# Kernel optimization log

Hardware: AMD Instinct MI355X
Metric: run time of the kernel (lower is better)

## Reference

```python
import jax, jax.numpy as jnp
import numpy as np

N_NODES = 50000


def gcn_conv(x, src, dst, W, b):
    # PyG GCNConv: h = D^-1/2 (A+I) D^-1/2 (x W) + b, aggregation at dst.
    n = x.shape[0]
    deg = jax.ops.segment_sum(jnp.ones_like(dst, dtype=x.dtype), dst, num_segments=n)
    dinv = jnp.where(deg > 0, jax.lax.rsqrt(deg), 0.0)
    norm = dinv[src] * dinv[dst]                      # [E]
    h = x @ W                                         # [N, out]
    msg = h[src] * norm[:, None]                      # [E, out] gather
    out = jax.ops.segment_sum(msg, dst, num_segments=n)  # scatter-add
    return out + b


def setup_inputs() -> dict:
    key = jax.random.key(0)
    k1, k2, k3, k4 = jax.random.split(key, 4)
    in_dim, hid, out_dim = 128, 256, 128
    x = jax.random.normal(k1, (N_NODES, in_dim), dtype=jnp.float32)
    edge_index = jax.random.randint(k2, (2, 800000), 0, N_NODES, dtype=jnp.int64)
    s1 = 1.0 / np.sqrt(in_dim)
    s2 = 1.0 / np.sqrt(hid)
    W1 = jax.random.uniform(k3, (in_dim, hid), jnp.float32, -s1, s1)
    b1 = jnp.zeros((hid,), jnp.float32)
    W2 = jax.random.uniform(k4, (hid, out_dim), jnp.float32, -s2, s2)
    b2 = jnp.zeros((out_dim,), jnp.float32)
    return {"x": x, "edge_index": edge_index, "W1": W1, "b1": b1, "W2": W2, "b2": b2}


def reference(x, edge_index, W1, b1, W2, b2):
    n = x.shape[0]
    loops = jnp.arange(n, dtype=edge_index.dtype)
    src = jnp.concatenate([edge_index[0], loops])  # add self-loops
    dst = jnp.concatenate([edge_index[1], loops])
    h = jax.nn.relu(gcn_conv(x, src, dst, W1, b1))
    # dropout in eval mode -> identity
    return gcn_conv(h, src, dst, W2, b2)
```

## Files before the change

### kernel.cpp

```cpp
#include <hip/hip_runtime.h>
#include <hip/hip_bf16.h>


typedef __bf16 bf16x8v __attribute__((ext_vector_type(8)));
typedef short  s16x8   __attribute__((ext_vector_type(8)));
typedef float  f32x4   __attribute__((ext_vector_type(4)));

#define IN_DIM 128
#define HID    256
#define OUTD   128
#define BKT_SHIFT 7
#define BKT_NODES 128
#define MAXB 512
#define CAP  8192
#define EBLK 512

__device__ __forceinline__ float2 bf2f(__hip_bfloat162 v) {
    return make_float2(__bfloat162float(v.x), __bfloat162float(v.y));
}
__device__ __forceinline__ __hip_bfloat162 f2bf(float a, float b) {
    __hip_bfloat162 r; r.x = __float2bfloat16(a); r.y = __float2bfloat16(b); return r;
}
__device__ __forceinline__ void acc_row(float* acc, s16x8 r) {
    __hip_bfloat162* p = (__hip_bfloat162*)&r;
#pragma unroll
    for (int j = 0; j < 4; ++j) {
        float2 f = bf2f(p[j]);
        acc[2 * j]     += f.x;
        acc[2 * j + 1] += f.y;
    }
}

__device__ __forceinline__ int detect_f32(const void* W2raw) {
    const unsigned short* u = (const unsigned short*)W2raw;
    int f32 = 0;
#pragma unroll
    for (int i = 0; i < 64; ++i) {
        unsigned e = (u[i] >> 7) & 0xFF;
        if (e >= 0x7F) f32 = 1;
    }
    return f32;
}


__device__ __forceinline__ short ldw(const void* raw, int idx, int f32) {
    if (f32) {
        __hip_bfloat16 h = __float2bfloat16(((const float*)raw)[idx]);
        return *(short*)&h;
    }
    return ((const short*)raw)[idx];
}

template <int K, int NN>
__device__ __forceinline__ void swz_one(const void* Wraw, int f32,
                                        short* __restrict__ Bsw, int tid) {
    constexpr int KC = K / 32;
    constexpr int NT = NN / 16;
    if (tid >= NT * KC * 64) return;
    int lane = tid & 63;
    int kc   = (tid >> 6) % KC;
    int nt   = tid / (64 * KC);
    int n  = nt * 16 + (lane & 15);
    int kb = kc * 32 + (lane >> 4) * 8;
    s16x8 v;
#pragma unroll
    for (int j = 0; j < 8; ++j) v[j] = ldw(Wraw, (kb + j) * NN + n, f32);
    ((s16x8*)Bsw)[tid] = v;
}

__global__ __launch_bounds__(256) void k_prep_w(
        const void* W1raw, const void* b1raw, const void* W2raw, const void* b2raw,
        const void* eiraw, short* __restrict__ Bsw1, short* __restrict__ Bsw2,
        __hip_bfloat16* __restrict__ b1c, __hip_bfloat16* __restrict__ b2c,
        int* __restrict__ flags) {
    int f32 = detect_f32(W2raw);
    int blk = blockIdx.x, t = threadIdx.x;
    if (blk < 16) {
        swz_one<IN_DIM, HID>(W1raw, f32, Bsw1, blk * 256 + t);
    } else if (blk < 32) {
        swz_one<HID, OUTD>(W2raw, f32, Bsw2, (blk - 16) * 256 + t);
    } else {
        short s1 = ldw(b1raw, t, f32);
        b1c[t] = *(__hip_bfloat16*)&s1;
        if (t < OUTD) {
            short s2 = ldw(b2raw, t, f32);
            b2c[t] = *(__hip_bfloat16*)&s2;
        }
        if (t == 0) {
            const unsigned* ip = (const unsigned*)eiraw;
            unsigned orodd = 0;
#pragma unroll
            for (int i = 0; i < 64; ++i) orodd |= ip[2 * i + 1];
            flags[0] = f32;
            flags[1] = (orodd == 0) ? 1 : 0;
        }
    }
}


__global__ __launch_bounds__(256) void k_edges(
        const void* __restrict__ ei_, int E, int N, int NB,
        const int* __restrict__ flags, int* __restrict__ bcnt,
        unsigned* __restrict__ ppack) {
    __shared__ int lhist[4][MAXB];
    __shared__ int lbase[4][MAXB];
    int wv = threadIdx.x >> 6;
    int i64 = flags[1];
    const long long* p64 = (const long long*)ei_;
    const int*       p32 = (const int*)ei_;
    int per = (E + gridDim.x - 1) / gridDim.x;
    int e0 = blockIdx.x * per, e1 = min(e0 + per, E);
    for (int i = threadIdx.x; i < NB; i += 256) {
        lhist[0][i] = 0; lhist[1][i] = 0; lhist[2][i] = 0; lhist[3][i] = 0;
    }
    __syncthreads();
    for (int e = e0 + threadIdx.x; e < e1; e += 256) {
        int d = i64 ? (int)p64[E + e] : p32[E + e];
        if ((unsigned)d >= (unsigned)N) d = 0;
        atomicAdd(&lhist[wv][((unsigned)d) >> BKT_SHIFT], 1);
    }
    __syncthreads();
    for (int i = threadIdx.x; i < NB; i += 256) {
        int c0 = lhist[0][i], c1 = lhist[1][i], c2 = lhist[2][i], c3 = lhist[3][i];
        int tot = c0 + c1 + c2 + c3;
        int g = tot ? atomicAdd(&bcnt[i], tot) : 0;
        lbase[0][i] = g;
        lbase[1][i] = g + c0;
        lbase[2][i] = g + c0 + c1;
        lbase[3][i] = g + c0 + c1 + c2;
        lhist[0][i] = 0; lhist[1][i] = 0; lhist[2][i] = 0; lhist[3][i] = 0;
    }
    __syncthreads();
    for (int e = e0 + threadIdx.x; e < e1; e += 256) {
        int d = i64 ? (int)p64[E + e] : p32[E + e];
        int s = i64 ? (int)p64[e]     : p32[e];
        if ((unsigned)d >= (unsigned)N) d = 0;
        if ((unsigned)s >= (unsigned)N) s = 0;
        int b = ((unsigned)d) >> BKT_SHIFT;
        int pos = lbase[wv][b] + atomicAdd(&lhist[wv][b], 1);
        if (pos < CAP)
            ppack[(size_t)b * CAP + pos] = ((unsigned)(d & (BKT_NODES - 1)) << 25) | (unsigned)s;
    }
}


__global__ __launch_bounds__(512) void k_bsort(const int* __restrict__ bcnt,
                                               const unsigned* __restrict__ ppack,
                                               int NB,
                                               int* __restrict__ csr, int* __restrict__ offsets,
                                               float* __restrict__ dinv, int N,
                                               const void* __restrict__ xraw,
                                               const int* __restrict__ flags,
                                               __hip_bfloat16* __restrict__ xs) {
    __shared__ int sb[MAXB];
    __shared__ int h[BKT_NODES], base[BKT_NODES], s[BKT_NODES];
    __shared__ float sdv[BKT_NODES];
    int b = blockIdx.x;
    int t = threadIdx.x;
    int c = (t < NB) ? min(bcnt[t], CAP) : 0;
    sb[t] = c;
    __syncthreads();
    for (int off = 1; off < MAXB; off <<= 1) {
        int u = (t >= off) ? sb[t - off] : 0;
        __syncthreads();
        sb[t] += u;
        __syncthreads();
    }
    int cnt   = min(bcnt[b], CAP);
    int ebase = sb[b] - cnt;
    if (b == NB - 1 && t == 0) offsets[N] = sb[b];
    const unsigned* pp = ppack + (size_t)b * CAP;
    if (t < BKT_NODES) h[t] = 0;
    __syncthreads();
    for (int e = t; e < cnt; e += 512) atomicAdd(&h[pp[e] >> 25], 1);
    __syncthreads();
    int v = (t < BKT_NODES) ? h[t] : 0;
    if (t < BKT_NODES) s[t] = v;
    __syncthreads();
    for (int off = 1; off < BKT_NODES; off <<= 1) {
        int u = (t < BKT_NODES && t >= off) ? s[t - off] : 0;
        __syncthreads();
        if (t < BKT_NODES) s[t] += u;
        __syncthreads();
    }
    if (t < BKT_NODES) {
        int excl = s[t] - v;
        base[t] = excl;
        int node = b * BKT_NODES + t;
        float dv = 0.f;
        if (node < N) {
            dv = rsqrtf((float)(v + 1));
            offsets[node] = ebase + excl;
            dinv[node] = dv;
        } else {
            dinv[node] = 0.f;
        }
        sdv[t] = dv;
        h[t] = 0;
    }
    __syncthreads();
    for (int e = t; e < cnt; e += 512) {
        unsigned pk = pp[e];
        int ld = pk >> 25;
        int pos = ebase + base[ld] + atomicAdd(&h[ld], 1);
        csr[pos] = (int)(pk & 0x1FFFFFFu);
    }
    int f32 = flags[0];
    if (!f32) {
        const s16x8* xg = (const s16x8*)xraw;
        s16x8* xo = (s16x8*)xs;
        for (int u = t; u < BKT_NODES * 16; u += 512) {
            int row = u >> 4;
            int node = b * BKT_NODES + row;
            float dv = sdv[row];
            s16x8 val = {0, 0, 0, 0, 0, 0, 0, 0};
            if (node < N) {
                s16x8 xin = xg[(size_t)node * 16 + (u & 15)];
                __hip_bfloat162* xp = (__hip_bfloat162*)&xin;
                __hip_bfloat162* vp = (__hip_bfloat162*)&val;
#pragma unroll
                for (int j = 0; j < 4; ++j) {
                    float2 f = bf2f(xp[j]);
                    vp[j] = f2bf(dv * f.x, dv * f.y);
                }
            }
            xo[(size_t)node * 16 + (u & 15)] = val;
        }
    } else {
        const float4* xg = (const float4*)xraw;
        __hip_bfloat162* xo = (__hip_bfloat162*)xs;
        for (int u = t; u < BKT_NODES * 32; u += 512) {
            int row = u >> 5;
            int node = b * BKT_NODES + row;
            float dv = sdv[row];
            __hip_bfloat162 v0 = f2bf(0.f, 0.f), v1 = v0;
            if (node < N) {
                float4 xin = xg[(size_t)node * 32 + (u & 31)];
                v0 = f2bf(dv * xin.x, dv * xin.y);
                v1 = f2bf(dv * xin.z, dv * xin.w);
            }
            xo[(size_t)node * 64 + (u & 31) * 2]     = v0;
            xo[(size_t)node * 64 + (u & 31) * 2 + 1] = v1;
        }
    }
}


__global__ __launch_bounds__(256) void k_agg1(
        const s16x8* __restrict__ xs8, const int* __restrict__ offsets,
        const int* __restrict__ csr, const float* __restrict__ dinv,
        s16x8* __restrict__ a8, int N, int Npad, int nwaves) {
    int gw   = blockIdx.x * 4 + (threadIdx.x >> 6);
    int lane = threadIdx.x & 63;
    int g = lane >> 4, li = lane & 15;
    for (int v = gw; v < Npad; v += nwaves) {
        if (v >= N) {
            if (g == 0) { s16x8 z = {0,0,0,0,0,0,0,0}; a8[(size_t)v * 16 + li] = z; }
            continue;
        }
        float acc[8];
#pragma unroll
        for (int j = 0; j < 8; ++j) acc[j] = 0.f;
        int o0 = offsets[v], o1 = offsets[v + 1];
        if (g == 0) acc_row(acc, xs8[(size_t)v * 16 + li]);
        int e = o0 + g;
        for (; e + 12 < o1; e += 16) {
            int s0 = csr[e], s1 = csr[e + 4], s2 = csr[e + 8], s3 = csr[e + 12];
            s16x8 r0 = xs8[(size_t)s0 * 16 + li];
            s16x8 r1 = xs8[(size_t)s1 * 16 + li];
            s16x8 r2 = xs8[(size_t)s2 * 16 + li];
            s16x8 r3 = xs8[(size_t)s3 * 16 + li];
            acc_row(acc, r0); acc_row(acc, r1); acc_row(acc, r2); acc_row(acc, r3);
        }
        for (; e < o1; e += 4) acc_row(acc, xs8[(size_t)csr[e] * 16 + li]);
#pragma unroll
        for (int j = 0; j < 8; ++j) {
            acc[j] += __shfl_xor(acc[j], 16, 64);
            acc[j] += __shfl_xor(acc[j], 32, 64);
        }
        if (g == 0) {
            float dv = dinv[v];
            s16x8 outv;
            __hip_bfloat162* op = (__hip_bfloat162*)&outv;
#pragma unroll
            for (int j = 0; j < 4; ++j) op[j] = f2bf(dv * acc[2 * j], dv * acc[2 * j + 1]);
            a8[(size_t)v * 16 + li] = outv;
        }
    }
}


__global__ __launch_bounds__(256) void k_gemm12(
        const __hip_bfloat16* __restrict__ A, const __hip_bfloat16* __restrict__ Bsw1,
        const __hip_bfloat16* __restrict__ b1c, const __hip_bfloat16* __restrict__ Bsw2,
        const float* __restrict__ dinv, __hip_bfloat16* __restrict__ h2s) {
    __shared__ __align__(16) __hip_bfloat16 hl[128 * HID];
    int wave = threadIdx.x >> 6, lane = threadIdx.x & 63;
    int quad = lane >> 4, l16 = lane & 15;
    int mw = wave * 32;
    int gm = blockIdx.x * 128 + mw;

    bf16x8v a1f[2][4];
#pragma unroll
    for (int st = 0; st < 2; ++st)
#pragma unroll
        for (int kc = 0; kc < 4; ++kc)
            a1f[st][kc] = *reinterpret_cast<const bf16x8v*>(
                A + (size_t)(gm + st * 16 + l16) * IN_DIM + kc * 32 + quad * 8);

    const bf16x8v* B1 = reinterpret_cast<const bf16x8v*>(Bsw1);
    for (int nt = 0; nt < HID / 16; ++nt) {
        f32x4 acc0 = {0.f, 0.f, 0.f, 0.f}, acc1 = {0.f, 0.f, 0.f, 0.f};
#pragma unroll
        for (int kc = 0; kc < 4; ++kc) {
            bf16x8v bfrag = B1[(nt * 4 + kc) * 64 + lane];
            acc0 = __builtin_amdgcn_mfma_f32_16x16x32_bf16(a1f[0][kc], bfrag, acc0, 0, 0, 0);
            acc1 = __builtin_amdgcn_mfma_f32_16x16x32_bf16(a1f[1][kc], bfrag, acc1, 0, 0, 0);
        }
        int col = nt * 16 + l16;
        int gcol = col >> 3, csub = col & 7;
        float bv = __bfloat162float(b1c[col]);
#pragma unroll
        for (int r = 0; r < 4; ++r) {
            float v0 = acc0[r] + bv; v0 = v0 > 0.f ? v0 : 0.f;
            float v1 = acc1[r] + bv; v1 = v1 > 0.f ? v1 : 0.f;
            int r0 = mw + quad * 4 + r;
            int r1 = mw + 16 + quad * 4 + r;
            ((__hip_bfloat16*)((char*)hl + (size_t)r0 * (HID * 2) + ((gcol ^ (r0 & 31)) << 4)))[csub] = __float2bfloat16(v0);
            ((__hip_bfloat16*)((char*)hl + (size_t)r1 * (HID * 2) + ((gcol ^ (r1 & 31)) << 4)))[csub] = __float2bfloat16(v1);
        }
    }

    bf16x8v a2f[2][8];
#pragma unroll
    for (int st = 0; st < 2; ++st)
#pragma unroll
        for (int kc = 0; kc < 8; ++kc) {
            int row = mw + st * 16 + l16;
            int g = (kc * 4 + quad) ^ (row & 31);
            a2f[st][kc] = *reinterpret_cast<const bf16x8v*>(
                (char*)hl + (size_t)row * (HID * 2) + ((size_t)g << 4));
        }
    const bf16x8v* B2 = reinterpret_cast<const bf16x8v*>(Bsw2);
    int rb0 = gm + quad * 4, rb1 = gm + 16 + quad * 4;
    float sc0[4], sc1[4];
#pragma unroll
    for (int r = 0; r < 4; ++r) { sc0[r] = dinv[rb0 + r]; sc1[r] = dinv[rb1 + r]; }
    for (int nt = 0; nt < OUTD / 16; ++nt) {
        f32x4 acc0 = {0.f, 0.f, 0.f, 0.f}, acc1 = {0.f, 0.f, 0.f, 0.f};
#pragma unroll
        for (int kc = 0; kc < 8; ++kc) {
            bf16x8v bfrag = B2[(nt * 8 + kc) * 64 + lane];
            acc0 = __builtin_amdgcn_mfma_f32_16x16x32_bf16(a2f[0][kc], bfrag, acc0, 0, 0, 0);
            acc1 = __builtin_amdgcn_mfma_f32_16x16x32_bf16(a2f[1][kc], bfrag, acc1, 0, 0, 0);
        }
        int col = nt * 16 + l16;
#pragma unroll
        for (int r = 0; r < 4; ++r) {
            h2s[(size_t)(rb0 + r) * OUTD + col] = __float2bfloat16(acc0[r] * sc0[r]);
            h2s[(size_t)(rb1 + r) * OUTD + col] = __float2bfloat16(acc1[r] * sc1[r]);
        }
    }
}


__global__ __launch_bounds__(256) void k_agg2(
        const s16x8* __restrict__ h8, const int* __restrict__ offsets,
        const int* __restrict__ csr, const float* __restrict__ dinv,
        const __hip_bfloat16* __restrict__ b2c, const int* __restrict__ flags,
        void* __restrict__ outraw, int N, int nwaves) {
    int gw   = blockIdx.x * 4 + (threadIdx.x >> 6);
    int lane = threadIdx.x & 63;
    int g = lane >> 4, li = lane & 15;
    int f32 = flags[0];
    float bb[8];
    {
        s16x8 bv = ((const s16x8*)b2c)[li];
        __hip_bfloat162* bp = (__hip_bfloat162*)&bv;
#pragma unroll
        for (int j = 0; j < 4; ++j) {
            float2 f = bf2f(bp[j]);
            bb[2 * j] = f.x; bb[2 * j + 1] = f.y;
        }
    }
    for (int v = gw; v < N; v += nwaves) {
        float acc[8];
#pragma unroll
        for (int j = 0; j < 8; ++j) acc[j] = 0.f;
        int o0 = offsets[v], o1 = offsets[v + 1];
        if (g == 0) acc_row(acc, h8[(size_t)v * 16 + li]);
        int e = o0 + g;
        for (; e + 12 < o1; e += 16) {
            int s0 = csr[e], s1 = csr[e + 4], s2 = csr[e + 8], s3 = csr[e + 12];
            s16x8 r0 = h8[(size_t)s0 * 16 + li];
            s16x8 r1 = h8[(size_t)s1 * 16 + li];
            s16x8 r2 = h8[(size_t)s2 * 16 + li];
            s16x8 r3 = h8[(size_t)s3 * 16 + li];
            acc_row(acc, r0); acc_row(acc, r1); acc_row(acc, r2); acc_row(acc, r3);
        }
        for (; e < o1; e += 4) acc_row(acc, h8[(size_t)csr[e] * 16 + li]);
#pragma unroll
        for (int j = 0; j < 8; ++j) {
            acc[j] += __shfl_xor(acc[j], 16, 64);
            acc[j] += __shfl_xor(acc[j], 32, 64);
        }
        if (g == 0) {
            float dv = dinv[v];
            if (f32) {
                float4* of = (float4*)outraw;
                float4 o0v = {dv * acc[0] + bb[0], dv * acc[1] + bb[1],
                              dv * acc[2] + bb[2], dv * acc[3] + bb[3]};
                float4 o1v = {dv * acc[4] + bb[4], dv * acc[5] + bb[5],
                              dv * acc[6] + bb[6], dv * acc[7] + bb[7]};
                of[(size_t)v * 32 + li * 2]     = o0v;
                of[(size_t)v * 32 + li * 2 + 1] = o1v;
            } else {
                s16x8 outv;
                __hip_bfloat162* op = (__hip_bfloat162*)&outv;
#pragma unroll
                for (int j = 0; j < 4; ++j)
                    op[j] = f2bf(dv * acc[2 * j] + bb[2 * j], dv * acc[2 * j + 1] + bb[2 * j + 1]);
                ((s16x8*)outraw)[(size_t)v * 16 + li] = outv;
            }
        }
    }
}


extern "C" void kernel_launch(void* const* d_in, const int* in_sizes, int n_in,
                              void* d_out, int out_size, void* d_ws, size_t ws_size,
                              hipStream_t stream) {
    const void* x  = d_in[0];
    const void* ei = d_in[1];
    const void* W1 = d_in[2];
    const void* b1 = d_in[3];
    const void* W2 = d_in[4];
    const void* b2 = d_in[5];

    const int N = in_sizes[0] / IN_DIM;
    const int E = in_sizes[1] / 2;
    const int Npad = ((N + 127) / 128) * 128;
    const int NB = Npad / BKT_NODES;

    char* w = (char*)d_ws;
    auto alloc = [&](size_t bytes) -> void* {
        void* p = (void*)w;
        w += (bytes + 255) / 256 * 256;
        return p;
    };
    int*   flags   = (int*)alloc(256);
    int*   bcnt    = (int*)alloc((size_t)MAXB * 4);
    int*   offsets = (int*)alloc((size_t)(N + 1) * 4);
    float* dinv    = (float*)alloc((size_t)Npad * 4);
    unsigned* ppack = (unsigned*)alloc((size_t)NB * CAP * 4);
    int*   csr     = (int*)alloc((size_t)E * 4);
    short* Bsw1 = (short*)alloc((size_t)IN_DIM * HID * 2);
    short* Bsw2 = (short*)alloc((size_t)HID * OUTD * 2);
    __hip_bfloat16* b1c = (__hip_bfloat16*)alloc((size_t)HID * 2);
    __hip_bfloat16* b2c = (__hip_bfloat16*)alloc((size_t)OUTD * 2);
    __hip_bfloat16* xs  = (__hip_bfloat16*)alloc((size_t)Npad * IN_DIM * 2);
    __hip_bfloat16* a1  = (__hip_bfloat16*)alloc((size_t)Npad * IN_DIM * 2);
    __hip_bfloat16* h2s = xs;

    k_prep_w<<<33, 256, 0, stream>>>(W1, b1, W2, b2, ei, Bsw1, Bsw2, b1c, b2c, flags);
    hipMemsetAsync(bcnt, 0, (size_t)MAXB * 4, stream);

    k_edges<<<EBLK, 256, 0, stream>>>(ei, E, N, NB, flags, bcnt, ppack);
    k_bsort<<<NB, 512, 0, stream>>>(bcnt, ppack, NB, csr, offsets, dinv, N,
                                    x, flags, xs);

    const int aggBlocks = 2048, nwaves = aggBlocks * 4;
    k_agg1<<<aggBlocks, 256, 0, stream>>>((const s16x8*)xs, offsets, csr, dinv,
                                          (s16x8*)a1, N, Npad, nwaves);

    k_gemm12<<<NB, 256, 0, stream>>>(a1, (const __hip_bfloat16*)Bsw1, b1c,
                                     (const __hip_bfloat16*)Bsw2, dinv, h2s);

    k_agg2<<<aggBlocks, 256, 0, stream>>>((const s16x8*)h2s, offsets, csr, dinv,
                                          b2c, flags, d_out, N, nwaves);
}
```

Before: 220.1 us.

## Split aggregation feature dim into column slices with one 4-lane group per node

Both aggregation kernels change their work mapping. Previously one wave handled a node, with four 16-lane groups splitting its edges and a shuffle reduction at the end. Now each block covers 64 nodes and one of four 32-column slices, so each node gets four lanes that each walk all its edges over a 16-byte chunk, and no cross-lane reduction is needed. The block index is swizzled so consecutive blocks pair up on adjacent node groups. The intent is to drop the shuffle reductions, the idle lanes in low-degree nodes and the persistent grid-stride loop. The cost is that each lane walks the full edge list serially and csr entries are read once per slice, and the block-index swizzle only handles feature-slice locality.

```diff
diff --git a/kernel.cpp b/kernel.cpp
--- a/kernel.cpp
+++ b/kernel.cpp
@@ -249,43 +249,108 @@
 __global__ __launch_bounds__(256) void k_agg1(
         const s16x8* __restrict__ xs8, const int* __restrict__ offsets,
         const int* __restrict__ csr, const float* __restrict__ dinv,
-        s16x8* __restrict__ a8, int N, int Npad, int nwaves) {
-    int gw   = blockIdx.x * 4 + (threadIdx.x >> 6);
-    int lane = threadIdx.x & 63;
-    int g = lane >> 4, li = lane & 15;
-    for (int v = gw; v < Npad; v += nwaves) {
-        if (v >= N) {
-            if (g == 0) { s16x8 z = {0,0,0,0,0,0,0,0}; a8[(size_t)v * 16 + li] = z; }
-            continue;
-        }
-        float acc[8];
-#pragma unroll
-        for (int j = 0; j < 8; ++j) acc[j] = 0.f;
-        int o0 = offsets[v], o1 = offsets[v + 1];
-        if (g == 0) acc_row(acc, xs8[(size_t)v * 16 + li]);
-        int e = o0 + g;
-        for (; e + 12 < o1; e += 16) {
-            int s0 = csr[e], s1 = csr[e + 4], s2 = csr[e + 8], s3 = csr[e + 12];
-            s16x8 r0 = xs8[(size_t)s0 * 16 + li];
-            s16x8 r1 = xs8[(size_t)s1 * 16 + li];
-            s16x8 r2 = xs8[(size_t)s2 * 16 + li];
-            s16x8 r3 = xs8[(size_t)s3 * 16 + li];
-            acc_row(acc, r0); acc_row(acc, r1); acc_row(acc, r2); acc_row(acc, r3);
-        }
-        for (; e < o1; e += 4) acc_row(acc, xs8[(size_t)csr[e] * 16 + li]);
-#pragma unroll
-        for (int j = 0; j < 8; ++j) {
-            acc[j] += __shfl_xor(acc[j], 16, 64);
-            acc[j] += __shfl_xor(acc[j], 32, 64);
-        }
-        if (g == 0) {
-            float dv = dinv[v];
-            s16x8 outv;
-            __hip_bfloat162* op = (__hip_bfloat162*)&outv;
-#pragma unroll
-            for (int j = 0; j < 4; ++j) op[j] = f2bf(dv * acc[2 * j], dv * acc[2 * j + 1]);
-            a8[(size_t)v * 16 + li] = outv;
-        }
+        s16x8* __restrict__ a8, int N, int Npad) {
+    int bid = blockIdx.x;
+    int slice = (bid & 7) >> 1;
+    int nb = ((bid >> 3) << 1) | (bid & 1);
+    int wave = threadIdx.x >> 6, lane = threadIdx.x & 63;
+    int sg = lane >> 2, lg = lane & 3;
+    int v  = nb * 64 + wave * 16 + sg;
+    int su = slice * 4 + lg;
+    if (v >= Npad) return;
+    if (v >= N) {
+        s16x8 z = {0, 0, 0, 0, 0, 0, 0, 0};
+        a8[(size_t)v * 16 + su] = z;
+        return;
+    }
+    float acc[8];
+    acc_row_init:;
+    {
+        s16x8 self = xs8[(size_t)v * 16 + su];
+        __hip_bfloat162* p = (__hip_bfloat162*)&self;
+#pragma unroll
+        for (int j = 0; j < 4; ++j) {
+            float2 f = bf2f(p[j]);
+            acc[2 * j] = f.x; acc[2 * j + 1] = f.y;
+        }
+    }
+    int e = offsets[v], o1 = offsets[v + 1];
+    for (; e + 3 < o1; e += 4) {
+        int s0 = csr[e], s1 = csr[e + 1], s2 = csr[e + 2], s3 = csr[e + 3];
+        s16x8 r0 = xs8[(size_t)s0 * 16 + su];
+        s16x8 r1 = xs8[(size_t)s1 * 16 + su];
+        s16x8 r2 = xs8[(size_t)s2 * 16 + su];
+        s16x8 r3 = xs8[(size_t)s3 * 16 + su];
+        acc_row(acc, r0); acc_row(acc, r1); acc_row(acc, r2); acc_row(acc, r3);
+    }
+    for (; e < o1; ++e) acc_row(acc, xs8[(size_t)csr[e] * 16 + su]);
+    float dv = dinv[v];
+    s16x8 outv;
+    __hip_bfloat162* op = (__hip_bfloat162*)&outv;
+#pragma unroll
+    for (int j = 0; j < 4; ++j) op[j] = f2bf(dv * acc[2 * j], dv * acc[2 * j + 1]);
+    a8[(size_t)v * 16 + su] = outv;
+}
+
+__global__ __launch_bounds__(256) void k_agg2(
+        const s16x8* __restrict__ h8, const int* __restrict__ offsets,
+        const int* __restrict__ csr, const float* __restrict__ dinv,
+        const __hip_bfloat16* __restrict__ b2c, const int* __restrict__ flags,
+        void* __restrict__ outraw, int N, int Npad) {
+    int bid = blockIdx.x;
+    int slice = (bid & 7) >> 1;
+    int nb = ((bid >> 3) << 1) | (bid & 1);
+    int wave = threadIdx.x >> 6, lane = threadIdx.x & 63;
+    int sg = lane >> 2, lg = lane & 3;
+    int v  = nb * 64 + wave * 16 + sg;
+    int su = slice * 4 + lg;
+    if (v >= N) return;
+    float acc[8];
+    {
+        s16x8 self = h8[(size_t)v * 16 + su];
+        __hip_bfloat162* p = (__hip_bfloat162*)&self;
+#pragma unroll
+        for (int j = 0; j < 4; ++j) {
+            float2 f = bf2f(p[j]);
+            acc[2 * j] = f.x; acc[2 * j + 1] = f.y;
+        }
+    }
+    int e = offsets[v], o1 = offsets[v + 1];
+    for (; e + 3 < o1; e += 4) {
+        int s0 = csr[e], s1 = csr[e + 1], s2 = csr[e + 2], s3 = csr[e + 3];
+        s16x8 r0 = h8[(size_t)s0 * 16 + su];
+        s16x8 r1 = h8[(size_t)s1 * 16 + su];
+        s16x8 r2 = h8[(size_t)s2 * 16 + su];
+        s16x8 r3 = h8[(size_t)s3 * 16 + su];
+        acc_row(acc, r0); acc_row(acc, r1); acc_row(acc, r2); acc_row(acc, r3);
+    }
+    for (; e < o1; ++e) acc_row(acc, h8[(size_t)csr[e] * 16 + su]);
+    float dv = dinv[v];
+    float bb[8];
+    {
+        s16x8 bv = ((const s16x8*)b2c)[su];
+        __hip_bfloat162* bp = (__hip_bfloat162*)&bv;
+#pragma unroll
+        for (int j = 0; j < 4; ++j) {
+            float2 f = bf2f(bp[j]);
+            bb[2 * j] = f.x; bb[2 * j + 1] = f.y;
+        }
+    }
+    if (flags[0]) {
+        float4* of = (float4*)outraw;
+        float4 o0v = {dv * acc[0] + bb[0], dv * acc[1] + bb[1],
+                      dv * acc[2] + bb[2], dv * acc[3] + bb[3]};
+        float4 o1v = {dv * acc[4] + bb[4], dv * acc[5] + bb[5],
+                      dv * acc[6] + bb[6], dv * acc[7] + bb[7]};
+        of[(size_t)v * 32 + su * 2]     = o0v;
+        of[(size_t)v * 32 + su * 2 + 1] = o1v;
+    } else {
+        s16x8 outv;
+        __hip_bfloat162* op = (__hip_bfloat162*)&outv;
+#pragma unroll
+        for (int j = 0; j < 4; ++j)
+            op[j] = f2bf(dv * acc[2 * j] + bb[2 * j], dv * acc[2 * j + 1] + bb[2 * j + 1]);
+        ((s16x8*)outraw)[(size_t)v * 16 + su] = outv;
     }
 }
 
@@ -359,69 +424,6 @@
         for (int r = 0; r < 4; ++r) {
             h2s[(size_t)(rb0 + r) * OUTD + col] = __float2bfloat16(acc0[r] * sc0[r]);
             h2s[(size_t)(rb1 + r) * OUTD + col] = __float2bfloat16(acc1[r] * sc1[r]);
-        }
-    }
-}
-
-
-__global__ __launch_bounds__(256) void k_agg2(
-        const s16x8* __restrict__ h8, const int* __restrict__ offsets,
-        const int* __restrict__ csr, const float* __restrict__ dinv,
-        const __hip_bfloat16* __restrict__ b2c, const int* __restrict__ flags,
-        void* __restrict__ outraw, int N, int nwaves) {
-    int gw   = blockIdx.x * 4 + (threadIdx.x >> 6);
-    int lane = threadIdx.x & 63;
-    int g = lane >> 4, li = lane & 15;
-    int f32 = flags[0];
-    float bb[8];
-    {
-        s16x8 bv = ((const s16x8*)b2c)[li];
-        __hip_bfloat162* bp = (__hip_bfloat162*)&bv;
-#pragma unroll
-        for (int j = 0; j < 4; ++j) {
-            float2 f = bf2f(bp[j]);
-            bb[2 * j] = f.x; bb[2 * j + 1] = f.y;
-        }
-    }
-    for (int v = gw; v < N; v += nwaves) {
-        float acc[8];
-#pragma unroll
-        for (int j = 0; j < 8; ++j) acc[j] = 0.f;
-        int o0 = offsets[v], o1 = offsets[v + 1];
-        if (g == 0) acc_row(acc, h8[(size_t)v * 16 + li]);
-        int e = o0 + g;
-        for (; e + 12 < o1; e += 16) {
-            int s0 = csr[e], s1 = csr[e + 4], s2 = csr[e + 8], s3 = csr[e + 12];
-            s16x8 r0 = h8[(size_t)s0 * 16 + li];
-            s16x8 r1 = h8[(size_t)s1 * 16 + li];
-            s16x8 r2 = h8[(size_t)s2 * 16 + li];
-            s16x8 r3 = h8[(size_t)s3 * 16 + li];
-            acc_row(acc, r0); acc_row(acc, r1); acc_row(acc, r2); acc_row(acc, r3);
-        }
-        for (; e < o1; e += 4) acc_row(acc, h8[(size_t)csr[e] * 16 + li]);
-#pragma unroll
-        for (int j = 0; j < 8; ++j) {
-            acc[j] += __shfl_xor(acc[j], 16, 64);
-            acc[j] += __shfl_xor(acc[j], 32, 64);
-        }
-        if (g == 0) {
-            float dv = dinv[v];
-            if (f32) {
-                float4* of = (float4*)outraw;
-                float4 o0v = {dv * acc[0] + bb[0], dv * acc[1] + bb[1],
-                              dv * acc[2] + bb[2], dv * acc[3] + bb[3]};
-                float4 o1v = {dv * acc[4] + bb[4], dv * acc[5] + bb[5],
-                              dv * acc[6] + bb[6], dv * acc[7] + bb[7]};
-                of[(size_t)v * 32 + li * 2]     = o0v;
-                of[(size_t)v * 32 + li * 2 + 1] = o1v;
-            } else {
-                s16x8 outv;
-                __hip_bfloat162* op = (__hip_bfloat162*)&outv;
-#pragma unroll
-                for (int j = 0; j < 4; ++j)
-                    op[j] = f2bf(dv * acc[2 * j] + bb[2 * j], dv * acc[2 * j + 1] + bb[2 * j + 1]);
-                ((s16x8*)outraw)[(size_t)v * 16 + li] = outv;
-            }
         }
     }
 }
@@ -469,13 +471,13 @@
     k_bsort<<<NB, 512, 0, stream>>>(bcnt, ppack, NB, csr, offsets, dinv, N,
                                     x, flags, xs);
 
-    const int aggBlocks = 2048, nwaves = aggBlocks * 4;
-    k_agg1<<<aggBlocks, 256, 0, stream>>>((const s16x8*)xs, offsets, csr, dinv,
-                                          (s16x8*)a1, N, Npad, nwaves);
+    const int aggGrid = (Npad / 64) * 4;
+    k_agg1<<<aggGrid, 256, 0, stream>>>((const s16x8*)xs, offsets, csr, dinv,
+                                        (s16x8*)a1, N, Npad);
 
     k_gemm12<<<NB, 256, 0, stream>>>(a1, (const __hip_bfloat16*)Bsw1, b1c,
                                      (const __hip_bfloat16*)Bsw2, dinv, h2s);
 
-    k_agg2<<<aggBlocks, 256, 0, stream>>>((const s16x8*)h2s, offsets, csr, dinv,
-                                          b2c, flags, d_out, N, nwaves);
-}
+    k_agg2<<<aggGrid, 256, 0, stream>>>((const s16x8*)h2s, offsets, csr, dinv,
+                                        b2c, flags, d_out, N, Npad);
+}
```

Result: slower. 231.2 us (+5.0%).
